# Kernel tuning notes

Hardware: AMD Instinct MI355X
Metric: run time of the kernel (lower is better)

Reference implementation:

```python
import jax, jax.numpy as jnp
import numpy as np

EPS = 1e-12

def _l2normalize(v):
    return v / (jnp.sum(v ** 2) ** 0.5 + EPS)

def spectral_norm(w, u):
    # w: [Cin, Cout] (flattened 1x1 conv kernel), u: [1, Cout]; 1 power iteration
    v = _l2normalize(u @ w.T)          # [1, Cin]
    u2 = _l2normalize(v @ w)           # [1, Cout]
    sigma = (v @ w @ u2.T)[0, 0]
    return w / sigma

def conv1x1(x, w):
    # x: [B,H,W,Cin], w: [Cin,Cout]
    return jnp.einsum('bhwc,cd->bhwd', x, w)

def maxpool2(x):
    B, H, W, C = x.shape
    return x.reshape(B, H // 2, 2, W // 2, 2, C).max(axis=(2, 4))

def setup_inputs() -> dict:
    key = jax.random.key(0)
    ks = jax.random.split(key, 10)
    B, H, W, C = 16, 64, 64, 512
    c8, c2 = C // 8, C // 2
    x = jax.random.normal(ks[0], (B, H, W, C), dtype=jnp.float32)
    k_theta = jax.random.normal(ks[1], (C, c8), dtype=jnp.float32) * 0.05
    u_theta = jax.random.normal(ks[2], (1, c8), dtype=jnp.float32)
    k_phi = jax.random.normal(ks[3], (C, c8), dtype=jnp.float32) * 0.05
    u_phi = jax.random.normal(ks[4], (1, c8), dtype=jnp.float32)
    k_g = jax.random.normal(ks[5], (C, c2), dtype=jnp.float32) * 0.05
    u_g = jax.random.normal(ks[6], (1, c2), dtype=jnp.float32)
    k_attn = jax.random.normal(ks[7], (c2, C), dtype=jnp.float32) * 0.05
    u_attn = jax.random.normal(ks[8], (1, C), dtype=jnp.float32)
    sigma = jnp.float32(0.1)
    return {"x": x, "k_theta": k_theta, "u_theta": u_theta,
            "k_phi": k_phi, "u_phi": u_phi, "k_g": k_g, "u_g": u_g,
            "k_attn": k_attn, "u_attn": u_attn, "sigma": sigma}

def reference(x, k_theta, u_theta, k_phi, u_phi, k_g, u_g, k_attn, u_attn, sigma):
    B, H, W, C = x.shape
    c8, c2 = C // 8, C // 2
    loc = H * W
    down = loc // 4
    theta = conv1x1(x, spectral_norm(k_theta, u_theta)).reshape(B, loc, c8)
    phi = maxpool2(conv1x1(x, spectral_norm(k_phi, u_phi))).reshape(B, down, c8)
    attn = jax.nn.softmax(jnp.einsum('bnc,bmc->bnm', theta, phi), axis=-1)  # [B, loc, down]
    g = maxpool2(conv1x1(x, spectral_norm(k_g, u_g))).reshape(B, down, c2)
    attn_g = jnp.einsum('bnm,bmc->bnc', attn, g).reshape(B, H, W, c2)
    attn_g = conv1x1(attn_g, spectral_norm(k_attn, u_attn))
    return x + sigma * attn_g
```

## Files before the change

kernel.cpp:

```cpp
#include <hip/hip_runtime.h>
#include <hip/hip_bf16.h>


using bf16 = __hip_bfloat16;
typedef unsigned short u16;
typedef __attribute__((ext_vector_type(8))) short bf16x8;
typedef __attribute__((ext_vector_type(4))) float f32x4;

#define MFMA16(a, b, c) __builtin_amdgcn_mfma_f32_16x16x32_bf16((a), (b), (c), 0, 0, 0)

#define WS_FLAG   0
#define WS_WAT2   787456
#define WS_THETA  1311744
#define WS_PHI    9700352
#define WS_G      11797504
#define WS_WAT    20186112
#define WS_TOTAL  20448256

__device__ __forceinline__ float bf2f(bf16 v) { return __bfloat162float(v); }
__device__ __forceinline__ bf16 f2bf(float v) { return __float2bfloat16(v); }
__device__ __forceinline__ u16 f2bf_bits(float v) { bf16 h = f2bf(v); return *(u16*)&h; }

template <typename T> struct io;
template <> struct io<bf16> {
  static __device__ __forceinline__ float ld(const bf16* p) { return bf2f(*p); }
  static __device__ __forceinline__ void st(bf16* p, float v) { *p = f2bf(v); }
  static __device__ __forceinline__ int tag() { return 0; }
};
template <> struct io<float> {
  static __device__ __forceinline__ float ld(const float* p) { return *p; }
  static __device__ __forceinline__ void st(float* p, float v) { *p = v; }
  static __device__ __forceinline__ int tag() { return 1; }
};

__global__ __launch_bounds__(256) void detect_kernel(const void* xraw, int* flag) {
  const uint4* p = (const uint4*)xraw;
  int t = threadIdx.x;
  int cnt = 0;
#pragma unroll 8
  for (int i = 0; i < 32; ++i) {
    uint4 v = p[t + i * 256];
    unsigned d[4] = {v.x, v.y, v.z, v.w};
#pragma unroll
    for (int k = 0; k < 4; ++k) {
      if ((d[k] & 0x7F80u) == 0x7F80u) cnt++;
      if ((d[k] & 0x7F800000u) == 0x7F800000u) cnt++;
    }
  }
#pragma unroll
  for (int o = 32; o > 0; o >>= 1) cnt += __shfl_down(cnt, o, 64);
  __shared__ int red[4];
  if ((t & 63) == 0) red[t >> 6] = cnt;
  __syncthreads();
  if (t == 0) flag[0] = (red[0] + red[1] + red[2] + red[3] > 4) ? 1 : 0;
}

__device__ __forceinline__ float block_sum_256(float x, float* red) {
#pragma unroll
  for (int o = 32; o > 0; o >>= 1) x += __shfl_down(x, o, 64);
  __syncthreads();
  if ((threadIdx.x & 63) == 0) red[threadIdx.x >> 6] = x;
  __syncthreads();
  return red[0] + red[1] + red[2] + red[3];
}

template <typename T, int CIN, int COUT, int MODE>
__device__ __forceinline__ void sn_impl(const T* w, const T* u,
                                        u16* wAllT, u16* waT) {
  __shared__ float v[CIN];
  __shared__ float red[4];
  const int t = threadIdx.x, wv = t >> 6, ln = t & 63;

  float uv[COUT / 64];
#pragma unroll
  for (int jj = 0; jj < COUT / 64; ++jj) uv[jj] = io<T>::ld(u + jj * 64 + ln);

#pragma unroll 2
  for (int i = wv; i < CIN; i += 4) {
    float acc = 0.f;
#pragma unroll
    for (int jj = 0; jj < COUT / 64; ++jj)
      acc += uv[jj] * io<T>::ld(w + (size_t)i * COUT + jj * 64 + ln);
#pragma unroll
    for (int o = 32; o > 0; o >>= 1) acc += __shfl_down(acc, o, 64);
    if (ln == 0) v[i] = acc;
  }
  __syncthreads();
  float loc = 0.f;
  for (int i = t; i < CIN; i += 256) loc += v[i] * v[i];
  float s1 = block_sum_256(loc, red);
  float inv1 = 1.f / (sqrtf(s1) + 1e-12f);

  float loc2 = 0.f;
#pragma unroll
  for (int j0 = 0; j0 < COUT; j0 += 256) {
    int j = j0 + t;
    if (j < COUT) {
      float a0 = 0.f, a1 = 0.f, a2 = 0.f, a3 = 0.f;
#pragma unroll 4
      for (int i = 0; i < CIN; i += 4) {
        a0 += v[i + 0] * io<T>::ld(w + (size_t)(i + 0) * COUT + j);
        a1 += v[i + 1] * io<T>::ld(w + (size_t)(i + 1) * COUT + j);
        a2 += v[i + 2] * io<T>::ld(w + (size_t)(i + 2) * COUT + j);
        a3 += v[i + 3] * io<T>::ld(w + (size_t)(i + 3) * COUT + j);
      }
      float acc = ((a0 + a1) + (a2 + a3)) * inv1;
      loc2 += acc * acc;
    }
  }
  float s2 = block_sum_256(loc2, red);
  float sigma = s2 / (sqrtf(s2) + 1e-12f);
  float winv = 1.f / sigma;

#pragma unroll 4
  for (int k = t; k < CIN * COUT; k += 256) {
    float val = io<T>::ld(w + k) * winv;
    u16 bits = f2bf_bits(val);
    int i = k / COUT, j = k % COUT;
    if constexpr (MODE == 0) wAllT[(size_t)j * 512 + i] = bits;
    if constexpr (MODE == 1) wAllT[(size_t)(64 + j) * 512 + i] = bits;
    if constexpr (MODE == 2) wAllT[(size_t)(128 + j) * 512 + i] = bits;
    if constexpr (MODE == 3) waT[(size_t)j * 256 + i] = bits;
  }
}

template <typename T>
__global__ __launch_bounds__(256) void sn_kernel(
    const void* ktv, const void* utv, const void* kpv, const void* upv,
    const void* kgv, const void* ugv, const void* kav, const void* uav,
    u16* wAllT, u16* waT, const int* flag) {
  if (flag[0] != io<T>::tag()) return;
  switch (blockIdx.x) {
    case 0:  sn_impl<T, 512, 64, 0>((const T*)ktv, (const T*)utv, wAllT, waT); break;
    case 1:  sn_impl<T, 512, 64, 1>((const T*)kpv, (const T*)upv, wAllT, waT); break;
    case 2:  sn_impl<T, 512, 256, 2>((const T*)kgv, (const T*)ugv, wAllT, waT); break;
    default: sn_impl<T, 256, 512, 3>((const T*)kav, (const T*)uav, wAllT, waT); break;
  }
}

template <typename T>
__global__ __launch_bounds__(256, 2) void conv3_mfma_kernel(
    const void* xv, const u16* __restrict__ wAllT,
    bf16* __restrict__ theta, bf16* __restrict__ phi, bf16* __restrict__ gT,
    const int* flag) {
  if (flag[0] != io<T>::tag()) return;
  constexpr bool SPLIT = sizeof(T) == 4;
  const T* x = (const T*)xv;

  __shared__ u16 xh_s[2][64][136];
  __shared__ u16 xl_s[2][64][136];

  const int tid = threadIdx.x;
  const int w = tid >> 6;
  const int lane = tid & 63;
  const int quad = lane >> 4;
  const int l15 = lane & 15;
  const int bb = blockIdx.x >> 6;
  const int tile = blockIdx.x & 63;
  const int pth = tile >> 3, ptw = tile & 7;

  const int sp = tid >> 2;
  const int sq = tid & 3;
  const int swin = sp >> 2, sd = sp & 3;
  const int sh = 2 * (pth * 4 + (swin >> 2)) + (sd >> 1);
  const int sw = 2 * (ptw * 4 + (swin & 3)) + (sd & 1);
  const T* xrow = x + ((size_t)(bb * 64 + sh) * 64 + sw) * 512 + sq * 32;

  auto STAGE = [&](int buf, int kc) {
    if constexpr (SPLIT) {
      const float* src = (const float*)xrow + kc * 128;
#pragma unroll
      for (int hl = 0; hl < 2; ++hl) {
        float f[16];
#pragma unroll
        for (int i = 0; i < 4; ++i) {
          float4 v4 = ((const float4*)src)[hl * 4 + i];
          f[4 * i] = v4.x; f[4 * i + 1] = v4.y; f[4 * i + 2] = v4.z; f[4 * i + 3] = v4.w;
        }
        unsigned ph_[8], pl_[8];
#pragma unroll
        for (int i = 0; i < 8; ++i) {
          float a = f[2 * i], b = f[2 * i + 1];
          u16 ha = f2bf_bits(a), hb = f2bf_bits(b);
          float ra = a - __uint_as_float((unsigned)ha << 16);
          float rb = b - __uint_as_float((unsigned)hb << 16);
          ph_[i] = (unsigned)ha | ((unsigned)hb << 16);
          pl_[i] = (unsigned)f2bf_bits(ra) | ((unsigned)f2bf_bits(rb) << 16);
        }
        *(uint4*)&xh_s[buf][sp][sq * 32 + hl * 16] =
            make_uint4(ph_[0], ph_[1], ph_[2], ph_[3]);
        *(uint4*)&xh_s[buf][sp][sq * 32 + hl * 16 + 8] =
            make_uint4(ph_[4], ph_[5], ph_[6], ph_[7]);
        *(uint4*)&xl_s[buf][sp][sq * 32 + hl * 16] =
            make_uint4(pl_[0], pl_[1], pl_[2], pl_[3]);
        *(uint4*)&xl_s[buf][sp][sq * 32 + hl * 16 + 8] =
            make_uint4(pl_[4], pl_[5], pl_[6], pl_[7]);
      }
    } else {
      const u16* src = (const u16*)xrow + kc * 128;
#pragma unroll
      for (int i = 0; i < 4; ++i)
        *(uint4*)&xh_s[buf][sp][sq * 32 + i * 8] = ((const uint4*)src)[i];
    }
  };

  f32x4 acc[4][6];
#pragma unroll
  for (int mt = 0; mt < 4; ++mt)
#pragma unroll
    for (int nt = 0; nt < 6; ++nt) acc[mt][nt] = (f32x4){0.f, 0.f, 0.f, 0.f};

  const u16* wb = wAllT + (size_t)(w * 96 + l15) * 512 + quad * 8;

  STAGE(0, 0);
  __syncthreads();
#pragma unroll 1
  for (int kc = 0; kc < 4; ++kc) {
    const int buf = kc & 1;
    if (kc < 3) STAGE(buf ^ 1, kc + 1);
#pragma unroll
    for (int ks = 0; ks < 4; ++ks) {
      bf16x8 ah[4], al[4];
#pragma unroll
      for (int mt = 0; mt < 4; ++mt) {
        ah[mt] = *(const bf16x8*)&xh_s[buf][mt * 16 + l15][ks * 32 + quad * 8];
        if constexpr (SPLIT)
          al[mt] = *(const bf16x8*)&xl_s[buf][mt * 16 + l15][ks * 32 + quad * 8];
      }
#pragma unroll
      for (int nt = 0; nt < 6; ++nt) {
        bf16x8 b = *(const bf16x8*)(wb + (size_t)nt * 16 * 512 + kc * 128 + ks * 32);
#pragma unroll
        for (int mt = 0; mt < 4; ++mt) {
          acc[mt][nt] = MFMA16(ah[mt], b, acc[mt][nt]);
          if constexpr (SPLIT) acc[mt][nt] = MFMA16(al[mt], b, acc[mt][nt]);
        }
      }
    }
    __syncthreads();
  }

#pragma unroll
  for (int nt = 0; nt < 6; ++nt) {
    const int nb = w * 96 + nt * 16;
    const int n = nb + l15;
    if (nb < 64) {
#pragma unroll
      for (int mt = 0; mt < 4; ++mt)
#pragma unroll
        for (int r = 0; r < 4; ++r) {
          int p = mt * 16 + quad * 4 + r;
          int win = p >> 2, d = p & 3;
          int h = 2 * (pth * 4 + (win >> 2)) + (d >> 1);
          int wc = 2 * (ptw * 4 + (win & 3)) + (d & 1);
          theta[((size_t)bb * 4096 + h * 64 + wc) * 64 + n] = f2bf(acc[mt][nt][r]);
        }
    } else if (nb < 128) {
      const int ch = n - 64;
#pragma unroll
      for (int mt = 0; mt < 4; ++mt) {
        int win = mt * 4 + quad;
        int pp = (pth * 4 + (win >> 2)) * 32 + (ptw * 4 + (win & 3));
        float mx = fmaxf(fmaxf(acc[mt][nt][0], acc[mt][nt][1]),
                         fmaxf(acc[mt][nt][2], acc[mt][nt][3]));
        phi[((size_t)bb * 1024 + pp) * 64 + ch] = f2bf(mx);
      }
    } else {
      const int ch = n - 128;
#pragma unroll
      for (int mt = 0; mt < 4; ++mt) {
        int win = mt * 4 + quad;
        int pp = (pth * 4 + (win >> 2)) * 32 + (ptw * 4 + (win & 3));
        float mx = fmaxf(fmaxf(acc[mt][nt][0], acc[mt][nt][1]),
                         fmaxf(acc[mt][nt][2], acc[mt][nt][3]));
        gT[((size_t)bb * 256 + ch) * 1024 + pp] = f2bf(mx);
      }
    }
  }
}

template <typename T>
__global__ __launch_bounds__(256) void attn_kernel(
    const bf16* __restrict__ thetab, const bf16* __restrict__ phib,
    const bf16* __restrict__ gTb, void* __restrict__ outv, const int* flag) {
  if (flag[0] != io<T>::tag()) return;
  __shared__ u16 ph_s[32][66];
  __shared__ u16 gt_s[256][34];
  __shared__ u16 p_s[4][16][34];

  const int tid = threadIdx.x;
  const int w = tid >> 6;
  const int lane = tid & 63;
  const int quad = lane >> 4;
  const int l15 = lane & 15;
  const int qt = blockIdx.x * 4 + w;
  const int bb = qt >> 8;
  const int q0 = (qt & 255) * 16;

  const u16* th = (const u16*)thetab + ((size_t)bb * 4096 + q0 + l15) * 64 + quad * 8;
  const bf16x8 a0 = *(const bf16x8*)th;
  const bf16x8 a1 = *(const bf16x8*)(th + 32);

  const u16* ph = (const u16*)phib + (size_t)bb * 1024 * 64;
  const u16* gT = (const u16*)gTb + (size_t)bb * 256 * 1024;

  f32x4 o[16];
#pragma unroll
  for (int i = 0; i < 16; ++i) o[i] = (f32x4){0.f, 0.f, 0.f, 0.f};
  float mold[4] = {-1e30f, -1e30f, -1e30f, -1e30f};
  float lsum[4] = {0.f, 0.f, 0.f, 0.f};

  const int pr = tid >> 3, pc = (tid & 7) * 8;
  const int gr = tid >> 2, gq = (tid & 3) * 8;

  uint4 pf_p, pf_g[4];
  auto LOAD = [&](int kc) {
    pf_p = *(const uint4*)(ph + ((kc * 32 + pr) * 64 + pc));
#pragma unroll
    for (int i = 0; i < 4; ++i)
      pf_g[i] = *(const uint4*)(gT + (size_t)(i * 64 + gr) * 1024 + kc * 32 + gq);
  };
  LOAD(0);

#pragma unroll 1
  for (int kc = 0; kc < 32; ++kc) {
    __syncthreads();
    *(uint4*)&ph_s[pr][pc] = pf_p;
#pragma unroll
    for (int i = 0; i < 4; ++i)
      *(uint4*)&gt_s[i * 64 + gr][gq] = pf_g[i];
    __syncthreads();
    if (kc < 31) LOAD(kc + 1);

    f32x4 s[2];
#pragma unroll
    for (int t4 = 0; t4 < 2; ++t4) {
      bf16x8 b0 = *(const bf16x8*)&ph_s[t4 * 16 + l15][quad * 8];
      bf16x8 b1 = *(const bf16x8*)&ph_s[t4 * 16 + l15][32 + quad * 8];
      f32x4 z = (f32x4){0.f, 0.f, 0.f, 0.f};
      z = MFMA16(a0, b0, z);
      z = MFMA16(a1, b1, z);
      s[t4] = z;
    }
    float rmax[4], alpha[4], rsum[4];
    bool need = false;
#pragma unroll
    for (int r = 0; r < 4; ++r) {
      rmax[r] = fmaxf(s[0][r], s[1][r]);
#pragma unroll
      for (int m = 1; m <= 8; m <<= 1) rmax[r] = fmaxf(rmax[r], __shfl_xor(rmax[r], m, 64));
      bool upd = rmax[r] > mold[r] + 8.f;
      alpha[r] = upd ? __expf(mold[r] - rmax[r]) : 1.f;
      if (upd) mold[r] = rmax[r];
      need |= upd;
      rsum[r] = 0.f;
    }
#pragma unroll
    for (int t4 = 0; t4 < 2; ++t4)
#pragma unroll
      for (int r = 0; r < 4; ++r) {
        float pv = __expf(s[t4][r] - mold[r]);
        rsum[r] += pv;
        p_s[w][quad * 4 + r][t4 * 16 + l15] = f2bf_bits(pv);
      }
#pragma unroll
    for (int r = 0; r < 4; ++r)
#pragma unroll
      for (int m = 1; m <= 8; m <<= 1) rsum[r] += __shfl_xor(rsum[r], m, 64);
    if (__any(need)) {
#pragma unroll
      for (int i = 0; i < 16; ++i) {
        o[i][0] *= alpha[0]; o[i][1] *= alpha[1];
        o[i][2] *= alpha[2]; o[i][3] *= alpha[3];
      }
#pragma unroll
      for (int r = 0; r < 4; ++r) lsum[r] = lsum[r] * alpha[r] + rsum[r];
    } else {
#pragma unroll
      for (int r = 0; r < 4; ++r) lsum[r] += rsum[r];
    }
    bf16x8 pa = *(const bf16x8*)&p_s[w][l15][quad * 8];
#pragma unroll
    for (int t4 = 0; t4 < 16; ++t4) {
      bf16x8 b = *(const bf16x8*)&gt_s[t4 * 16 + l15][quad * 8];
      o[t4] = MFMA16(pa, b, o[t4]);
    }
  }

  const size_t RB = 512 * sizeof(T);
  char* ob = (char*)outv;
  float inv[4];
#pragma unroll
  for (int r = 0; r < 4; ++r) inv[r] = 1.f / lsum[r];
#pragma unroll
  for (int t4 = 0; t4 < 16; ++t4)
#pragma unroll
    for (int r = 0; r < 4; ++r) {
      size_t row = (size_t)bb * 4096 + q0 + quad * 4 + r;
      u16* dst = (u16*)(ob + row * RB + RB / 2) + t4 * 16 + l15;
      *dst = f2bf_bits(o[t4][r] * inv[r]);
    }
}

template <typename T>
__global__ __launch_bounds__(256, 3) void proj_kernel(
    const u16* __restrict__ waT, const void* __restrict__ xv,
    const void* __restrict__ sigv, void* __restrict__ outv, const int* flag) {
  if (flag[0] != io<T>::tag()) return;
  const T* xp = (const T*)xv;
  T* outp = (T*)outv;
  __shared__ u16 a_s[64][264];

  const int tid = threadIdx.x;
  const int w = tid >> 6;
  const int lane = tid & 63;
  const int quad = lane >> 4;
  const int l15 = lane & 15;
  const int R0 = blockIdx.x * 64;
  const size_t RB = 512 * sizeof(T);

  {
    int row = tid >> 2, seg = tid & 3;
    const uint4* src = (const uint4*)((const char*)outv + (size_t)(R0 + row) * RB + RB / 2);
#pragma unroll
    for (int i = 0; i < 8; ++i)
      *(uint4*)&a_s[row][seg * 64 + i * 8] = src[seg * 8 + i];
  }
  __syncthreads();

  float sg = io<T>::ld((const T*)sigv);
#pragma unroll 1
  for (int h = 0; h < 2; ++h) {
    f32x4 pc[16];
#pragma unroll
    for (int i = 0; i < 16; ++i) pc[i] = (f32x4){0.f, 0.f, 0.f, 0.f};
#pragma unroll 1
    for (int ks = 0; ks < 8; ++ks) {
      bf16x8 a = *(const bf16x8*)&a_s[w * 16 + l15][ks * 32 + quad * 8];
#pragma unroll
      for (int t4 = 0; t4 < 16; ++t4) {
        bf16x8 b = *(const bf16x8*)(waT + (size_t)(h * 256 + t4 * 16 + l15) * 256 + ks * 32 + quad * 8);
        pc[t4] = MFMA16(a, b, pc[t4]);
      }
    }
#pragma unroll
    for (int t4 = 0; t4 < 16; ++t4)
#pragma unroll
      for (int r = 0; r < 4; ++r) {
        int row = R0 + w * 16 + quad * 4 + r;
        int col = h * 256 + t4 * 16 + l15;
        size_t off = (size_t)row * 512 + col;
        io<T>::st(outp + off, io<T>::ld(xp + off) + sg * pc[t4][r]);
      }
  }
}

extern "C" void kernel_launch(void* const* d_in, const int* in_sizes, int n_in,
                              void* d_out, int out_size, void* d_ws, size_t ws_size,
                              hipStream_t stream) {
  if (ws_size < (size_t)WS_TOTAL) return;
  char* ws = (char*)d_ws;
  int*   flag  = (int*)(ws + WS_FLAG);
  u16*   wAllT = (u16*)(ws + WS_WAT2);
  bf16*  theta = (bf16*)(ws + WS_THETA);
  bf16*  phi   = (bf16*)(ws + WS_PHI);
  bf16*  gT    = (bf16*)(ws + WS_G);
  u16*   waT   = (u16*)(ws + WS_WAT);

  detect_kernel<<<1, 256, 0, stream>>>(d_in[0], flag);

  sn_kernel<bf16><<<4, 256, 0, stream>>>(d_in[1], d_in[2], d_in[3], d_in[4],
                                         d_in[5], d_in[6], d_in[7], d_in[8],
                                         wAllT, waT, flag);
  sn_kernel<float><<<4, 256, 0, stream>>>(d_in[1], d_in[2], d_in[3], d_in[4],
                                          d_in[5], d_in[6], d_in[7], d_in[8],
                                          wAllT, waT, flag);

  conv3_mfma_kernel<bf16><<<1024, 256, 0, stream>>>(d_in[0], wAllT, theta, phi, gT, flag);
  conv3_mfma_kernel<float><<<1024, 256, 0, stream>>>(d_in[0], wAllT, theta, phi, gT, flag);

  attn_kernel<bf16><<<1024, 256, 0, stream>>>(theta, phi, gT, d_out, flag);
  attn_kernel<float><<<1024, 256, 0, stream>>>(theta, phi, gT, d_out, flag);

  proj_kernel<bf16><<<1024, 256, 0, stream>>>(waT, d_in[0], d_in[9], d_out, flag);
  proj_kernel<float><<<1024, 256, 0, stream>>>(waT, d_in[0], d_in[9], d_out, flag);
}
```

Before: 881.8 us.

## Double attention key tile to 64 and drop register prefetch in attn kernel

The attention kernel now processes 64 keys per iteration instead of 32, halving the number of loop iterations, barriers and online-softmax rescale steps. It also removes the register-level prefetch of the next tile, so global loads are issued synchronously between barriers. Shared memory roughly doubles, which may lower occupancy, and load latency is no longer hidden behind compute.

```diff
diff --git a/kernel.cpp b/kernel.cpp
--- a/kernel.cpp
+++ b/kernel.cpp
@@ -284,9 +284,9 @@
     const bf16* __restrict__ thetab, const bf16* __restrict__ phib,
     const bf16* __restrict__ gTb, void* __restrict__ outv, const int* flag) {
   if (flag[0] != io<T>::tag()) return;
-  __shared__ u16 ph_s[32][66];
-  __shared__ u16 gt_s[256][34];
-  __shared__ u16 p_s[4][16][34];
+  __shared__ u16 ph_s[64][68];
+  __shared__ u16 gt_s[256][68];
+  __shared__ u16 p_s[4][16][68];
 
   const int tid = threadIdx.x;
   const int w = tid >> 6;
@@ -310,31 +310,27 @@
   float mold[4] = {-1e30f, -1e30f, -1e30f, -1e30f};
   float lsum[4] = {0.f, 0.f, 0.f, 0.f};
 
-  const int pr = tid >> 3, pc = (tid & 7) * 8;
-  const int gr = tid >> 2, gq = (tid & 3) * 8;
-
-  uint4 pf_p, pf_g[4];
-  auto LOAD = [&](int kc) {
-    pf_p = *(const uint4*)(ph + ((kc * 32 + pr) * 64 + pc));
-#pragma unroll
-    for (int i = 0; i < 4; ++i)
-      pf_g[i] = *(const uint4*)(gT + (size_t)(i * 64 + gr) * 1024 + kc * 32 + gq);
-  };
-  LOAD(0);
+  const int pr = tid >> 2, pc = (tid & 3) * 16;
+  const int gr = tid >> 3, gc = (tid & 7) * 8;
 
 #pragma unroll 1
-  for (int kc = 0; kc < 32; ++kc) {
+  for (int kc = 0; kc < 16; ++kc) {
     __syncthreads();
-    *(uint4*)&ph_s[pr][pc] = pf_p;
-#pragma unroll
-    for (int i = 0; i < 4; ++i)
-      *(uint4*)&gt_s[i * 64 + gr][gq] = pf_g[i];
+    {
+      const u16* src = ph + ((kc * 64 + pr) * 64 + pc);
+      *(uint4*)&ph_s[pr][pc] = *(const uint4*)src;
+      *(uint4*)&ph_s[pr][pc + 8] = *(const uint4*)(src + 8);
+    }
+#pragma unroll
+    for (int i = 0; i < 8; ++i) {
+      const u16* src = gT + (size_t)(i * 32 + gr) * 1024 + kc * 64 + gc;
+      *(uint4*)&gt_s[i * 32 + gr][gc] = *(const uint4*)src;
+    }
     __syncthreads();
-    if (kc < 31) LOAD(kc + 1);
-
-    f32x4 s[2];
-#pragma unroll
-    for (int t4 = 0; t4 < 2; ++t4) {
+
+    f32x4 s[4];
+#pragma unroll
+    for (int t4 = 0; t4 < 4; ++t4) {
       bf16x8 b0 = *(const bf16x8*)&ph_s[t4 * 16 + l15][quad * 8];
       bf16x8 b1 = *(const bf16x8*)&ph_s[t4 * 16 + l15][32 + quad * 8];
       f32x4 z = (f32x4){0.f, 0.f, 0.f, 0.f};
@@ -346,7 +342,7 @@
     bool need = false;
 #pragma unroll
     for (int r = 0; r < 4; ++r) {
-      rmax[r] = fmaxf(s[0][r], s[1][r]);
+      rmax[r] = fmaxf(fmaxf(s[0][r], s[1][r]), fmaxf(s[2][r], s[3][r]));
 #pragma unroll
       for (int m = 1; m <= 8; m <<= 1) rmax[r] = fmaxf(rmax[r], __shfl_xor(rmax[r], m, 64));
       bool upd = rmax[r] > mold[r] + 8.f;
@@ -356,7 +352,7 @@
       rsum[r] = 0.f;
     }
 #pragma unroll
-    for (int t4 = 0; t4 < 2; ++t4)
+    for (int t4 = 0; t4 < 4; ++t4)
 #pragma unroll
       for (int r = 0; r < 4; ++r) {
         float pv = __expf(s[t4][r] - mold[r]);
@@ -379,11 +375,14 @@
 #pragma unroll
       for (int r = 0; r < 4; ++r) lsum[r] += rsum[r];
     }
-    bf16x8 pa = *(const bf16x8*)&p_s[w][l15][quad * 8];
+    bf16x8 pa0 = *(const bf16x8*)&p_s[w][l15][quad * 8];
+    bf16x8 pa1 = *(const bf16x8*)&p_s[w][l15][32 + quad * 8];
 #pragma unroll
     for (int t4 = 0; t4 < 16; ++t4) {
-      bf16x8 b = *(const bf16x8*)&gt_s[t4 * 16 + l15][quad * 8];
-      o[t4] = MFMA16(pa, b, o[t4]);
+      bf16x8 b0 = *(const bf16x8*)&gt_s[t4 * 16 + l15][quad * 8];
+      bf16x8 b1 = *(const bf16x8*)&gt_s[t4 * 16 + l15][32 + quad * 8];
+      o[t4] = MFMA16(pa0, b0, o[t4]);
+      o[t4] = MFMA16(pa1, b1, o[t4]);
     }
   }
 
```

After: 739.7 us. 1.19x faster.
